# Optimization experiments

Hardware: AMD Instinct MI355X
Metric: run time of the kernel (lower is better)

The kernel has to match this reference:

```python
import jax, jax.numpy as jnp
import numpy as np

HEADS = 16

def _layernorm_LC(x, eps=1e-05):
    # Normalizes jointly over the last TWO dims (L, C), matching the custom LayerNorm.
    mean = jnp.mean(x, axis=(-2, -1), keepdims=True)
    var = jnp.mean((x - mean) ** 2, axis=(-2, -1), keepdims=True) + eps
    return (x - mean) / jnp.sqrt(var)  # affine is identity (ones/zeros)


def setup_inputs() -> dict:
    key = jax.random.key(0)
    ks = jax.random.split(key, 11)
    B, L, D = 2, 2048, 1024
    H = 4 * D
    s = 0.02
    return {
        'x': jax.random.normal(ks[0], (B, L, D), jnp.float32),
        'wq': jax.random.normal(ks[1], (D, D), jnp.float32) * s,
        'bq': jax.random.normal(ks[2], (D,), jnp.float32) * s,
        'wk': jax.random.normal(ks[3], (D, D), jnp.float32) * s,
        'bk': jax.random.normal(ks[4], (D,), jnp.float32) * s,
        'wv': jax.random.normal(ks[5], (D, D), jnp.float32) * s,
        'bv': jax.random.normal(ks[6], (D,), jnp.float32) * s,
        'w1': jax.random.normal(ks[7], (D, H), jnp.float32) * s,
        'b1': jax.random.normal(ks[8], (H,), jnp.float32) * s,
        'w2': jax.random.normal(ks[9], (H, D), jnp.float32) * s,
        'b2': jax.random.normal(ks[10], (D,), jnp.float32) * s,
    }


def reference(x, wq, bq, wk, bk, wv, bv, w1, b1, w2, b2):
    B, L, D = x.shape
    dh = D // HEADS
    # QKV projections
    q = (x @ wq + bq).reshape(B, L, HEADS, dh)
    k = (x @ wk + bk).reshape(B, L, HEADS, dh)
    v = (x @ wv + bv).reshape(B, L, HEADS, dh)
    # batched multi-head attention (equivalent to the per-head Python loop)
    scale = 1.0 / jnp.sqrt(jnp.float32(dh))
    scores = jnp.einsum('blhd,bmhd->bhlm', q, k) * scale
    attn = jax.nn.softmax(scores, axis=-1)
    out = jnp.einsum('bhlm,bmhd->blhd', attn, v).reshape(B, L, D)
    # residual + (L,C) layernorm
    h = _layernorm_LC(x + out)
    # feedforward (dropout is identity in eval)
    ff = jax.nn.relu(h @ w1 + b1) @ w2 + b2
    return _layernorm_LC(h + ff)
```

## Files before the change

### kernel.cpp

```cpp
#include <hip/hip_runtime.h>
#include <hip/hip_bf16.h>

typedef __hip_bfloat16 bf16;
typedef __attribute__((ext_vector_type(8))) short short8;
typedef __attribute__((ext_vector_type(4))) short short4v;
typedef __attribute__((ext_vector_type(4))) float f32x4;

#define CB 2
#define CL 2048
#define CD 1024
#define CH 4096
#define NHEADS 16
#define DH 64

__device__ __forceinline__ short f2bs(float f) {
    __hip_bfloat16 h = __float2bfloat16(f);
    return *reinterpret_cast<short*>(&h);
}
__device__ __forceinline__ float bs2f(short s) {
    __hip_bfloat16 h = *reinterpret_cast<__hip_bfloat16*>(&s);
    return __bfloat162float(h);
}

__device__ __forceinline__ void async_copy16(const short* g, short* l) {
    __builtin_amdgcn_global_load_lds((const __attribute__((address_space(1))) unsigned int*)g,
                                     (__attribute__((address_space(3))) unsigned int*)l,
                                     16, 0, 0);
}

__global__ void pack_bias_kernel(const float* __restrict__ bq, const float* __restrict__ bk,
                                 const float* __restrict__ bv, float* __restrict__ o,
                                 float* __restrict__ stats) {
    int i = blockIdx.x * 256 + threadIdx.x;
    if (i < 16) stats[i] = 0.0f;
    if (i < 3072) o[i] = i < 1024 ? bq[i] : (i < 2048 ? bk[i - 1024] : bv[i - 2048]);
}

__global__ void cvt_x_kernel(const float* __restrict__ x, short* __restrict__ o) {
    const int i = (blockIdx.x * 256 + threadIdx.x) * 4;
    const float4 v = *(const float4*)&x[i];
    short4v s; s[0] = f2bs(v.x); s[1] = f2bs(v.y); s[2] = f2bs(v.z); s[3] = f2bs(v.w);
    *(short4v*)&o[i] = s;
}

__global__ void transpose_cvt(const float* __restrict__ in, short* __restrict__ out,
                              int K, int N, int row_off) {
    __shared__ float T[32][33];
    const int tx = threadIdx.x & 31, ty = threadIdx.x >> 5;
    const int k0 = blockIdx.y * 32, n0 = blockIdx.x * 32;
    #pragma unroll
    for (int i = 0; i < 4; ++i)
        T[ty + i * 8][tx] = in[(size_t)(k0 + ty + i * 8) * N + n0 + tx];
    __syncthreads();
    #pragma unroll
    for (int i = 0; i < 4; ++i)
        out[(size_t)(row_off + n0 + ty + i * 8) * K + k0 + tx] = f2bs(T[tx][ty + i * 8]);
}

__global__ void transpose_qkv(const float* __restrict__ wq, const float* __restrict__ wk,
                              const float* __restrict__ wv, short* __restrict__ out) {
    __shared__ float T[32][33];
    const int z = blockIdx.z;
    const float* in = z == 0 ? wq : (z == 1 ? wk : wv);
    const int row_off = z * 1024;
    const int tx = threadIdx.x & 31, ty = threadIdx.x >> 5;
    const int k0 = blockIdx.y * 32, n0 = blockIdx.x * 32;
    #pragma unroll
    for (int i = 0; i < 4; ++i)
        T[ty + i * 8][tx] = in[(size_t)(k0 + ty + i * 8) * CD + n0 + tx];
    __syncthreads();
    #pragma unroll
    for (int i = 0; i < 4; ++i)
        out[(size_t)(row_off + n0 + ty + i * 8) * CD + k0 + tx] = f2bs(T[tx][ty + i * 8]);
}

template <int BN, int BK, int RELU, int EPI, int DB>
__launch_bounds__(256)
__global__ void gemm_mfma(const short* __restrict__ A,
                          const short* __restrict__ Bt,
                          const float* __restrict__ bias,
                          short* __restrict__ C,
                          short* __restrict__ C2,
                          int M, int N, int K,
                          float* __restrict__ stats) {
    constexpr int NT = BN / 32;
    constexpr int KH = BK / 32;
    constexpr int ACH = 16 * BK;
    constexpr int BCH = BN * BK / 8;
    constexpr int ASZ = 128 * BK;
    constexpr int BSZ = BN * BK;
    __shared__ short As[(DB ? 2 : 1) * ASZ];
    __shared__ short Bs[(DB ? 2 : 1) * BSZ];
    __shared__ float red[8];

    const int tid = threadIdx.x;
    const int wave = tid >> 6, lane = tid & 63, quad = lane >> 4, lm = lane & 15;
    const int wm = (wave & 1) * 64, wn = (wave >> 1) * (NT * 16);

    const int id = blockIdx.y * gridDim.x + blockIdx.x;
    const int xcd = id & 7, within = id >> 3;
    const int by = xcd * 4 + (within & 3);
    const int bx = within >> 2;
    const int row0 = by * 128, col0 = bx * BN;

    f32x4 acc[4][NT];
    #pragma unroll
    for (int i = 0; i < 4; ++i)
        #pragma unroll
        for (int j = 0; j < NT; ++j) { f32x4 z = {0.f, 0.f, 0.f, 0.f}; acc[i][j] = z; }

    auto stage = [&](int k0, int buf) {
        #pragma unroll
        for (int t = 0; t < ACH / 256; ++t) {
            const int c = t * 256 + tid;
            const int slab = c >> 9, idx = c & 511;
            const int r = idx >> 2, seg = idx & 3;
            async_copy16(A + (size_t)(row0 + r) * K + k0 + slab * 32 + seg * 8,
                         &As[buf * ASZ + c * 8]);
        }
        #pragma unroll
        for (int t = 0; t < BCH / 256; ++t) {
            const int c = t * 256 + tid;
            const int slab = c / (BN * 4), idx = c % (BN * 4);
            const int r = idx >> 2, seg = idx & 3;
            async_copy16(Bt + (size_t)(col0 + r) * K + k0 + slab * 32 + seg * 8,
                         &Bs[buf * BSZ + c * 8]);
        }
    };

    int cur = 0;
    if (DB) {
        stage(0, 0);
        __syncthreads();
    }

    for (int k0 = 0; k0 < K; k0 += BK) {
        if (DB) {
            if (k0 + BK < K) stage(k0 + BK, cur ^ 1);
        } else {
            stage(k0, 0);
            __syncthreads();
        }
        const short* Ap = &As[cur * ASZ];
        const short* Bp = &Bs[cur * BSZ];

        #pragma unroll
        for (int kh = 0; kh < KH; ++kh) {
            short8 af[4], bfr[NT];
            #pragma unroll
            for (int mt = 0; mt < 4; ++mt)
                af[mt] = *(const short8*)&Ap[kh * 4096 + (wm + mt * 16 + lm) * 32 + quad * 8];
            #pragma unroll
            for (int nt = 0; nt < NT; ++nt)
                bfr[nt] = *(const short8*)&Bp[kh * (BN * 32) + (wn + nt * 16 + lm) * 32 + quad * 8];
            #pragma unroll
            for (int mt = 0; mt < 4; ++mt)
                #pragma unroll
                for (int nt = 0; nt < NT; ++nt)
                    acc[mt][nt] = __builtin_amdgcn_mfma_f32_16x16x32_bf16(af[mt], bfr[nt], acc[mt][nt], 0, 0, 0);
        }
        __syncthreads();
        if (DB) cur ^= 1;
    }

    float s1 = 0.f, s2 = 0.f;
    #pragma unroll
    for (int mt = 0; mt < 4; ++mt) {
        #pragma unroll
        for (int nt = 0; nt < NT; ++nt) {
            const int col = col0 + wn + nt * 16 + lm;
            const float bv = bias[col];
            const int rowb = row0 + wm + mt * 16 + quad * 4;
            if (EPI == 1 && col >= 2048) {
                const int b = row0 >> 11;
                const int l0 = rowb & (CL - 1);
                const int lp = (l0 & ~63) | (l0 & 32) | ((l0 & 12) << 1) | ((l0 & 16) >> 2);
                short4v sv;
                #pragma unroll
                for (int r = 0; r < 4; ++r) sv[r] = f2bs(acc[mt][nt][r] + bv);
                *(short4v*)&C2[(size_t)b * CD * CL + (size_t)(col - 2048) * CL + lp] = sv;
            } else {
                #pragma unroll
                for (int r = 0; r < 4; ++r) {
                    float v = acc[mt][nt][r] + bv;
                    if (RELU) v = fmaxf(v, 0.f);
                    const int ld = (EPI == 1) ? 2048 : N;
                    const size_t idx = (size_t)(rowb + r) * ld + col;
                    if (EPI == 2) {
                        v += bs2f(C[idx]);
                        s1 += v; s2 += v * v;
                    }
                    C[idx] = f2bs(v);
                }
            }
        }
    }
    if (EPI == 2) {
        #pragma unroll
        for (int off = 1; off <= 32; off <<= 1) {
            s1 += __shfl_xor(s1, off, 64);
            s2 += __shfl_xor(s2, off, 64);
        }
        if (lane == 0) { red[wave] = s1; red[4 + wave] = s2; }
        __syncthreads();
        if (tid == 0) {
            const int batch = row0 >> 11;
            atomicAdd(&stats[batch * 2 + 0], red[0] + red[1] + red[2] + red[3]);
            atomicAdd(&stats[batch * 2 + 1], red[4] + red[5] + red[6] + red[7]);
        }
    }
}

__launch_bounds__(512)
__global__ void attn_mfma(const short* __restrict__ qk,
                          const short* __restrict__ vT,
                          const float* __restrict__ x,
                          short* __restrict__ sbuf,
                          float* __restrict__ stats) {
    __shared__ short Ks[2][64 * 64];
    __shared__ short Vs[2][64 * 64];
    __shared__ float red[16];

    const int tid = threadIdx.x;
    const int wave = tid >> 6, lane = tid & 63, quad = lane >> 4, lm = lane & 15;
    const int sx = lm & 7;

    const int id = blockIdx.z * (16 * 16) + blockIdx.y * 16 + blockIdx.x;
    const int xcd = id & 7, rest = id >> 3;
    const int qx = rest & 15, gq = rest >> 4;
    const int g = gq * 8 + xcd;
    const int h = g & 15, b = g >> 4;

    const int hoff = h * DH;
    const size_t rowb = (size_t)b * CL;
    const size_t vbase = (size_t)b * CD * CL + (size_t)hoff * CL;
    const int qbase0 = qx * 128 + wave * 16;

    short8 bq[2];
    #pragma unroll
    for (int kf = 0; kf < 2; ++kf)
        bq[kf] = *(const short8*)(qk + (rowb + qbase0 + lm) * 2048 + hoff + kf * 32 + quad * 8);

    f32x4 oacc[4];
    #pragma unroll
    for (int mt = 0; mt < 4; ++mt) { f32x4 z = {0.f, 0.f, 0.f, 0.f}; oacc[mt] = z; }
    float lsum = 0.f;

    auto stage = [&](int buf, int kt) {
        {
            const int key = tid >> 3, sp = tid & 7;
            async_copy16(qk + (rowb + kt * 64 + key) * 2048 + 1024 + hoff + ((sp ^ (key & 7)) * 8),
                         &Ks[buf][tid * 8]);
        }
        {
            const int row = tid >> 3, sp = tid & 7;
            async_copy16(vT + vbase + (size_t)row * CL + kt * 64 + ((sp ^ (row & 7)) * 8),
                         &Vs[buf][tid * 8]);
        }
    };

    stage(0, 0);
    __syncthreads();
    int cur = 0;

    for (int kt = 0; kt < CL / 64; ++kt) {
        if (kt + 1 < CL / 64) stage(cur ^ 1, kt + 1);
        const short* K_ = &Ks[cur][0];
        const short* V_ = &Vs[cur][0];

        float st[4][4];
        #pragma unroll
        for (int ktile = 0; ktile < 4; ++ktile) {
            const int krow = ktile * 16 + lm;
            const int s0 = (quad ^ sx) << 3;
            const short8 a0 = *(const short8*)&K_[krow * 64 + s0];
            const short8 a1 = *(const short8*)&K_[krow * 64 + (s0 ^ 32)];
            f32x4 s = {0.f, 0.f, 0.f, 0.f};
            __builtin_amdgcn_s_setprio(1);
            s = __builtin_amdgcn_mfma_f32_16x16x32_bf16(a0, bq[0], s, 0, 0, 0);
            s = __builtin_amdgcn_mfma_f32_16x16x32_bf16(a1, bq[1], s, 0, 0, 0);
            __builtin_amdgcn_s_setprio(0);
            #pragma unroll
            for (int r = 0; r < 4; ++r) {
                const float p = __expf(s[r] * 0.125f);
                lsum += p;
                st[ktile][r] = p;
            }
        }

        #pragma unroll
        for (int p = 0; p < 2; ++p) {
            short8 pf;
            #pragma unroll
            for (int r = 0; r < 4; ++r) {
                pf[r]     = f2bs(st[2 * p][r]);
                pf[4 + r] = f2bs(st[2 * p + 1][r]);
            }
            #pragma unroll
            for (int mt = 0; mt < 4; ++mt) {
                const int sc = (p * 4 + quad) ^ sx;
                const short8 vf = *(const short8*)&V_[(mt * 16 + lm) * 64 + sc * 8];
                __builtin_amdgcn_s_setprio(1);
                oacc[mt] = __builtin_amdgcn_mfma_f32_16x16x32_bf16(vf, pf, oacc[mt], 0, 0, 0);
                __builtin_amdgcn_s_setprio(0);
            }
        }
        __syncthreads();
        cur ^= 1;
    }

    lsum += __shfl_xor(lsum, 16, 64);
    lsum += __shfl_xor(lsum, 32, 64);

    float s1 = 0.f, s2 = 0.f;
    {
        const float inv = 1.0f / lsum;
        const size_t grow = rowb + qbase0 + lm;
        #pragma unroll
        for (int mt = 0; mt < 4; ++mt) {
            const size_t base = grow * CD + hoff + mt * 16 + quad * 4;
            const float4 xv = *(const float4*)&x[base];
            const float xa[4] = {xv.x, xv.y, xv.z, xv.w};
            short4v sv;
            #pragma unroll
            for (int r = 0; r < 4; ++r) {
                const float s = xa[r] + oacc[mt][r] * inv;
                s1 += s; s2 += s * s;
                sv[r] = f2bs(s);
            }
            *(short4v*)&sbuf[base] = sv;
        }
    }
    #pragma unroll
    for (int off = 1; off <= 32; off <<= 1) {
        s1 += __shfl_xor(s1, off, 64);
        s2 += __shfl_xor(s2, off, 64);
    }
    if (lane == 0) { red[wave] = s1; red[8 + wave] = s2; }
    __syncthreads();
    if (tid == 0) {
        float t1 = 0.f, t2 = 0.f;
        #pragma unroll
        for (int w = 0; w < 8; ++w) { t1 += red[w]; t2 += red[8 + w]; }
        atomicAdd(&stats[b * 2 + 0], t1);
        atomicAdd(&stats[b * 2 + 1], t2);
    }
}

template <typename TO>
__global__ void ln_apply(const short* __restrict__ s, const float* __restrict__ stats,
                         TO* __restrict__ out, int perBatch) {
    const int bId = blockIdx.y;
    const size_t base = (size_t)bId * perBatch;
    const float n = (float)perBatch;
    const float mean = stats[bId * 2 + 0] / n;
    const float var  = stats[bId * 2 + 1] / n - mean * mean + 1e-5f;
    const float inv  = rsqrtf(var);
    const int stride = gridDim.x * 256 * 8;
    for (int i = (blockIdx.x * 256 + threadIdx.x) * 8; i < perBatch; i += stride) {
        const short8 v8 = *(const short8*)&s[base + i];
        float o[8];
        #pragma unroll
        for (int j = 0; j < 8; ++j) o[j] = (bs2f(v8[j]) - mean) * inv;
        if (sizeof(TO) == 4) {
            float4 f0 = {o[0], o[1], o[2], o[3]}, f1 = {o[4], o[5], o[6], o[7]};
            *(float4*)&((float*)out)[base + i] = f0;
            *(float4*)&((float*)out)[base + i + 4] = f1;
        } else {
            short8 r;
            #pragma unroll
            for (int j = 0; j < 8; ++j) r[j] = f2bs(o[j]);
            *(short8*)&((short*)out)[base + i] = r;
        }
    }
}

extern "C" void kernel_launch(void* const* d_in, const int* in_sizes, int n_in,
                              void* d_out, int out_size, void* d_ws, size_t ws_size,
                              hipStream_t stream) {
    const float* x  = (const float*)d_in[0];
    const float* wq = (const float*)d_in[1];
    const float* bq = (const float*)d_in[2];
    const float* wk = (const float*)d_in[3];
    const float* bk = (const float*)d_in[4];
    const float* wv = (const float*)d_in[5];
    const float* bv = (const float*)d_in[6];
    const float* w1 = (const float*)d_in[7];
    const float* b1 = (const float*)d_in[8];
    const float* w2 = (const float*)d_in[9];
    const float* b2 = (const float*)d_in[10];

    const int BL = CB * CL;
    const int perBatch = CL * CD;

    char* ws = (char*)d_ws;
    const size_t MB = 1024 * 1024;
    short* Wqkvt = (short*)(ws);
    float* bqkv  = (float*)(ws + 6 * MB);
    short* w1t   = (short*)(ws);
    short* w2t   = (short*)(ws);
    short* xbf   = (short*)(ws + 8 * MB);
    short* qkb   = (short*)(ws + 16 * MB);
    short* vT    = (short*)(ws + 32 * MB);
    short* ff1   = (short*)(ws + 8 * MB);
    short* hbuf  = (short*)(ws + 40 * MB);
    float* stats = (float*)(ws + 48 * MB);

    dim3 blk(256);

    pack_bias_kernel<<<12, blk, 0, stream>>>(bq, bk, bv, bqkv, stats);
    cvt_x_kernel<<<BL * CD / 1024, blk, 0, stream>>>(x, xbf);
    transpose_qkv<<<dim3(32, 32, 3), blk, 0, stream>>>(wq, wk, wv, Wqkvt);

    gemm_mfma<128, 64, 0, 1, 0><<<dim3(3072 / 128, BL / 128), blk, 0, stream>>>(
        xbf, Wqkvt, bqkv, qkb, vT, BL, 3072, CD, nullptr);

    attn_mfma<<<dim3(CL / 128, NHEADS, CB), dim3(512), 0, stream>>>(qkb, vT, x, hbuf, stats);

    ln_apply<bf16><<<dim3(128, CB), blk, 0, stream>>>(hbuf, stats, (bf16*)hbuf, perBatch);

    transpose_cvt<<<dim3(128, 32), blk, 0, stream>>>(w1, w1t, CD, CH, 0);
    gemm_mfma<128, 64, 1, 0, 0><<<dim3(CH / 128, BL / 128), blk, 0, stream>>>(
        hbuf, w1t, b1, ff1, nullptr, BL, CH, CD, nullptr);

    transpose_cvt<<<dim3(32, 128), blk, 0, stream>>>(w2, w2t, CH, CD, 0);
    gemm_mfma<64, 64, 0, 2, 1><<<dim3(CD / 64, BL / 128), blk, 0, stream>>>(
        ff1, w2t, b2, hbuf, nullptr, BL, CD, CH, stats + 8);

    ln_apply<float><<<dim3(128, CB), blk, 0, stream>>>(hbuf, stats + 8, (float*)d_out, perBatch);
}
```

Measured before the change: 345.6 us.

## Replace double-buffered GEMM staging with a three-stage async pipeline using vmcnt waits

Turns the GEMM's double-buffered LDS staging into a triple-buffered pipeline that prefetches two K-tiles ahead. Explicit s_waitcnt vmcnt counts replace the full-drain syncthreads, so each iteration waits only for the tile about to be used. The aim is to hide more global-load latency behind the MFMA work. In exchange it uses more LDS, which can lower occupancy, and the hardcoded vmcnt counts assume a fixed number of async copies per stage.

```diff
diff --git a/kernel.cpp b/kernel.cpp
--- a/kernel.cpp
+++ b/kernel.cpp
@@ -74,7 +74,7 @@
         out[(size_t)(row_off + n0 + ty + i * 8) * CD + k0 + tx] = f2bs(T[tx][ty + i * 8]);
 }
 
-template <int BN, int BK, int RELU, int EPI, int DB>
+template <int BN, int BK, int RELU, int EPI, int PIPE>
 __launch_bounds__(256)
 __global__ void gemm_mfma(const short* __restrict__ A,
                           const short* __restrict__ Bt,
@@ -89,8 +89,9 @@
     constexpr int BCH = BN * BK / 8;
     constexpr int ASZ = 128 * BK;
     constexpr int BSZ = BN * BK;
-    __shared__ short As[(DB ? 2 : 1) * ASZ];
-    __shared__ short Bs[(DB ? 2 : 1) * BSZ];
+    constexpr int NBUF = PIPE ? 3 : 1;
+    __shared__ short As[NBUF * ASZ];
+    __shared__ short Bs[NBUF * BSZ];
     __shared__ float red[8];
 
     const int tid = threadIdx.x;
@@ -128,22 +129,7 @@
         }
     };
 
-    int cur = 0;
-    if (DB) {
-        stage(0, 0);
-        __syncthreads();
-    }
-
-    for (int k0 = 0; k0 < K; k0 += BK) {
-        if (DB) {
-            if (k0 + BK < K) stage(k0 + BK, cur ^ 1);
-        } else {
-            stage(k0, 0);
-            __syncthreads();
-        }
-        const short* Ap = &As[cur * ASZ];
-        const short* Bp = &Bs[cur * BSZ];
-
+    auto compute = [&](const short* Ap, const short* Bp) {
         #pragma unroll
         for (int kh = 0; kh < KH; ++kh) {
             short8 af[4], bfr[NT];
@@ -159,8 +145,36 @@
                 for (int nt = 0; nt < NT; ++nt)
                     acc[mt][nt] = __builtin_amdgcn_mfma_f32_16x16x32_bf16(af[mt], bfr[nt], acc[mt][nt], 0, 0, 0);
         }
-        __syncthreads();
-        if (DB) cur ^= 1;
+    };
+
+    if (PIPE) {
+        const int nt = K / BK;
+        stage(0, 0);
+        stage(BK, 1);
+        int cb = 0;
+        for (int it = 0; it < nt; ++it) {
+            if (it + 2 < nt) {
+                int pb = cb + 2; if (pb >= 3) pb -= 3;
+                stage((it + 2) * BK, pb);
+            }
+            if (it < nt - 2)       asm volatile("s_waitcnt vmcnt(12)" ::: "memory");
+            else if (it == nt - 2) asm volatile("s_waitcnt vmcnt(6)" ::: "memory");
+            else                   asm volatile("s_waitcnt vmcnt(0)" ::: "memory");
+            __builtin_amdgcn_sched_barrier(0);
+            __builtin_amdgcn_s_barrier();
+            __builtin_amdgcn_sched_barrier(0);
+            compute(&As[cb * ASZ], &Bs[cb * BSZ]);
+            __builtin_amdgcn_sched_barrier(0);
+            __builtin_amdgcn_s_barrier();
+            if (++cb == 3) cb = 0;
+        }
+    } else {
+        for (int k0 = 0; k0 < K; k0 += BK) {
+            stage(k0, 0);
+            __syncthreads();
+            compute(As, Bs);
+            __syncthreads();
+        }
     }
 
     float s1 = 0.f, s2 = 0.f;
```

After: 349.2 us. About the same (+1.1%).
